# Optimization experiments

Measured on AMD Instinct MI355X. Metric: run time of the kernel, lower is better.

Reference implementation:

```python
import jax, jax.numpy as jnp
import numpy as np

B, DIM, IN_DIM, H, W = 4, 256, 128, 128, 128
DD = IN_DIM // 2          # down_dim = 64
HEADS = 8
BN_EPS = 1e-5


def conv2d(x, w, b=None, pad=0, dil=1):
    y = jax.lax.conv_general_dilated(
        x, w, window_strides=(1, 1),
        padding=[(pad, pad), (pad, pad)],
        rhs_dilation=(dil, dil),
        dimension_numbers=('NCHW', 'OIHW', 'NCHW'))
    if b is not None:
        y = y + b[None, :, None, None]
    return y


def bn_relu(x, s, o):
    # eval-mode BatchNorm2d with running_mean=0, running_var=1
    return jax.nn.relu(x * (s / np.sqrt(1.0 + BN_EPS))[None, :, None, None] + o[None, :, None, None])


def setup_inputs() -> dict:
    ks = iter(jax.random.split(jax.random.key(0), 80))

    def w(shape, sc=0.05):
        return sc * jax.random.normal(next(ks), shape, jnp.float32)

    def s(c):
        return 1.0 + 0.1 * jax.random.normal(next(ks), (c,), jnp.float32)

    def o(c):
        return 0.02 * jax.random.normal(next(ks), (c,), jnp.float32)

    d = {}
    d['x'] = jax.random.normal(next(ks), (B, DIM, H, W), jnp.float32)
    d['w_dc'] = w((IN_DIM, DIM, 3, 3)); d['b_dc'] = w((IN_DIM,)); d['s_dc'] = s(IN_DIM); d['o_dc'] = o(IN_DIM)
    d['w1'] = w((DD, IN_DIM, 1, 1)); d['b1'] = w((DD,)); d['s1'] = s(DD); d['o1'] = o(DD)
    d['w2'] = w((DD, DD, 3, 3)); d['b2'] = w((DD,)); d['s2'] = s(DD); d['o2'] = o(DD)
    d['w3'] = w((DD, DD, 3, 3)); d['b3'] = w((DD,)); d['s3'] = s(DD); d['o3'] = o(DD)
    d['w4'] = w((DD, DD, 3, 3)); d['b4'] = w((DD,)); d['s4'] = s(DD); d['o4'] = o(DD)
    d['w5'] = w((DD, IN_DIM, 1, 1)); d['b5'] = w((DD,)); d['s5'] = s(DD); d['o5'] = o(DD)
    d['temperature'] = jnp.ones((HEADS, 1, 1), jnp.float32)
    d['w_po'] = w((DD, 2 * DD, 1, 1))  # project_out, bias=False
    d['w_wa'] = w((DD // 16, DD, 1, 1)); d['b_wa'] = w((DD // 16,)); d['s_wa'] = s(DD // 16); d['o_wa'] = o(DD // 16)
    d['w_wb'] = w((DD, DD // 16, 1, 1)); d['b_wb'] = w((DD,))
    d['w_f'] = w((DD, 5 * DD, 1, 1)); d['b_f'] = w((DD,)); d['s_f'] = s(DD); d['o_f'] = o(DD)
    d['w_oa'] = w((DD // 2, DD, 3, 3)); d['b_oa'] = w((DD // 2,)); d['s_oa'] = s(DD // 2); d['o_oa'] = o(DD // 2)
    d['w_ob'] = w((1, DD // 2, 1, 1)); d['b_ob'] = w((1,))
    return d


def reference(x, w_dc, b_dc, s_dc, o_dc, w1, b1, s1, o1, w2, b2, s2, o2,
              w3, b3, s3, o3, w4, b4, s4, o4, w5, b5, s5, o5,
              temperature, w_po, w_wa, b_wa, s_wa, o_wa, w_wb, b_wb,
              w_f, b_f, s_f, o_f, w_oa, b_oa, s_oa, o_oa, w_ob, b_ob):

    def branch(c):
        b, ch, h, wd = c.shape
        f = jnp.fft.fft2(c)                                   # [b,ch,h,w] complex64 (q=k=v=tepqkv)
        qkv = f.reshape(b, HEADS, ch // HEADS, h * wd)        # v (unnormalized)
        n = jnp.sqrt(jnp.sum(jnp.square(jnp.abs(qkv)), axis=-1, keepdims=True))
        qn = qkv / jnp.maximum(n, 1e-12)                      # F.normalize(dim=-1); q == k
        attn = jnp.einsum('bhcn,bhdn->bhcd', qn, qn) * temperature
        # custom complex normalization: separate real/imag softmax
        attn = jax.lax.complex(jax.nn.softmax(attn.real, axis=-1),
                               jax.nn.softmax(attn.imag, axis=-1))
        of = jnp.abs(jnp.fft.ifft2(jnp.einsum('bhcd,bhdn->bhcn', attn, qkv)))  # ifft2 over (c, hw)
        of = of.reshape(b, ch, h, wd)
        g = jax.nn.sigmoid(conv2d(bn_relu(conv2d(f.real, w_wa, b_wa), s_wa, o_wa), w_wb, b_wb))
        ol = jnp.abs(jnp.fft.ifft2(g * f))                    # ifft2 over (h, w)
        return conv2d(jnp.concatenate([of, ol], axis=1), w_po) + c

    xd = bn_relu(conv2d(x, w_dc, b_dc, pad=1), s_dc, o_dc)
    c1 = bn_relu(conv2d(xd, w1, b1), s1, o1)
    c2 = bn_relu(conv2d(c1, w2, b2, pad=3, dil=3), s2, o2)
    F2 = branch(c2)
    c3 = bn_relu(conv2d(c1 + F2, w3, b3, pad=5, dil=5), s3, o3)
    F3 = branch(c3)
    c4 = bn_relu(conv2d(c1 + F3, w4, b4, pad=7, dil=7), s4, o4)
    F4 = branch(c4)
    # conv5: global avg pool -> 1x1 conv -> bilinear upsample of a 1x1 map == broadcast
    c5 = bn_relu(conv2d(jnp.mean(xd, axis=(2, 3), keepdims=True), w5, b5), s5, o5)
    c5 = jnp.broadcast_to(c5, (c5.shape[0], c5.shape[1], xd.shape[2], xd.shape[3]))
    fused = bn_relu(conv2d(jnp.concatenate([c1, F2, F3, F4, c5], axis=1), w_f, b_f), s_f, o_f)
    return conv2d(bn_relu(conv2d(fused, w_oa, b_oa, pad=1), s_oa, o_oa), w_ob, b_ob)
```

## Files before the change

### kernel.cpp

```cpp
#include <hip/hip_runtime.h>

#define S 16384
#define PI_F 3.14159265358979f

struct Ptrs { const float* p[43]; };

enum : int {
  O_SBDC=0, O_SB1=256, O_SB2=512, O_SB3=768, O_SB4=1024, O_SB5=1280,
  O_SBWA=1536, O_SBF=1792, O_SBOA=2048,
  O_M=2304, O_C5=2816, O_NRM=3072, O_GRAM=3328, O_ATT2=7424, O_BEFF=11520,
  O_WB=16384,
  O_PART=147456,
  O_H=180224,
  O_WP=442368,
  O_A=524288,
  O_FIN=8912896,
  O_CC=25690112,
  O_DRE=29884416, O_DIMG=34078720,
  O_ERE=38273024, O_EIM=42467328,
  O_G=46661632
};

typedef short bfrag __attribute__((ext_vector_type(8)));
typedef float ffrag __attribute__((ext_vector_type(4)));

__device__ __forceinline__ float bf2f(unsigned short u){
  union { unsigned int i; float f; } v; v.i = ((unsigned int)u) << 16; return v.f;
}
__device__ __forceinline__ unsigned short f2bf(float f){
  unsigned int x = __float_as_uint(f);
  unsigned int r = x + 0x7fffu + ((x >> 16) & 1u);
  return (unsigned short)(r >> 16);
}

__global__ void prep_sb_kernel(Ptrs P, float* ws){
  const float r = rsqrtf(1.0f + 1e-5f);
  int bi=0, si=0, oi=0, C=0, dst=0;
  switch (blockIdx.x){
    case 0: bi=2; si=3; oi=4; C=128; dst=O_SBDC; break;
    case 1: bi=6; si=7; oi=8; C=64; dst=O_SB1; break;
    case 2: bi=10; si=11; oi=12; C=64; dst=O_SB2; break;
    case 3: bi=14; si=15; oi=16; C=64; dst=O_SB3; break;
    case 4: bi=18; si=19; oi=20; C=64; dst=O_SB4; break;
    case 5: bi=22; si=23; oi=24; C=64; dst=O_SB5; break;
    case 6: bi=28; si=29; oi=30; C=4;  dst=O_SBWA; break;
    case 7: bi=34; si=35; oi=36; C=64; dst=O_SBF; break;
    default: bi=38; si=39; oi=40; C=32; dst=O_SBOA; break;
  }
  for (int c = threadIdx.x; c < C; c += 256){
    float bb = P.p[bi][c], ss = P.p[si][c], oo = P.p[oi][c];
    float sc = ss * r;
    ws[dst + c] = sc;
    ws[dst + C + c] = bb * sc + oo;
  }
}

__global__ __launch_bounds__(256) void xpad_kernel(const float* __restrict__ x,
    unsigned short* __restrict__ XT){
  int yy = blockIdx.x, b = blockIdx.y;
  long obase = ((long)(b*130) + yy) * (130L*256);
  int tid = threadIdx.x;
  if (yy == 0 || yy == 129){
    uint4 z; z.x=0; z.y=0; z.z=0; z.w=0;
    for (int i = tid; i < 130*256/8; i += 256)
      *(uint4*)(XT + obase + (long)i*8) = z;
    return;
  }
  __shared__ float LT[64][129];
  int y = yy - 1;
  for (int c0 = 0; c0 < 256; c0 += 64){
    for (int idx = tid; idx < 64*128; idx += 256){
      int ci = idx >> 7, xx = idx & 127;
      LT[ci][xx] = x[((long)(b*256 + c0 + ci)*128 + y)*128 + xx];
    }
    __syncthreads();
    for (int idx = tid; idx < 128*16; idx += 256){
      int xp = idx >> 4, c4 = (idx & 15)*4;
      ushort4 v;
      v.x = f2bf(LT[c4][xp]);   v.y = f2bf(LT[c4+1][xp]);
      v.z = f2bf(LT[c4+2][xp]); v.w = f2bf(LT[c4+3][xp]);
      *(ushort4*)(XT + obase + (long)(xp+1)*256 + c0 + c4) = v;
    }
    __syncthreads();
  }
  if (tid < 64){
    ushort4 z; z.x=0; z.y=0; z.z=0; z.w=0;
    *(ushort4*)(XT + obase + tid*4) = z;
    *(ushort4*)(XT + obase + 129L*256 + tid*4) = z;
  }
}

__global__ void wt_kernel(const float* __restrict__ w, unsigned short* __restrict__ WH,
    unsigned short* __restrict__ WL){
  for (int e = blockIdx.x*256 + threadIdx.x; e < 294912; e += gridDim.x*256){
    int c32 = e & 31, co = (e >> 5) & 127, kc = (e >> 12) & 7, sh = e >> 15;
    int ky = sh / 3, kx = sh - ky*3;
    int ci = kc*32 + c32;
    float v = w[((long)(co*256 + ci)*3 + ky)*3 + kx];
    unsigned short h = f2bf(v);
    WH[e] = h;
    WL[e] = f2bf(v - bf2f(h));
  }
}

__global__ void wtg_kernel(Ptrs P, unsigned short* __restrict__ WB){
  const float* w; int cout; long off;
  switch (blockIdx.y){
    case 0: w = P.p[9];  cout = 64; off = 0;      break;
    case 1: w = P.p[13]; cout = 64; off = 73728;  break;
    case 2: w = P.p[17]; cout = 64; off = 147456; break;
    default: w = P.p[37]; cout = 32; off = 221184; break;
  }
  int total = 576*cout;
  unsigned short* WH = WB + off;
  unsigned short* WL = WH + total;
  for (int e = blockIdx.x*256 + threadIdx.x; e < total; e += gridDim.x*256){
    int c32 = e & 31;
    int co = (e >> 5) & (cout - 1);
    int kc = (e / (32*cout)) & 1;
    int sh = e / (64*cout);
    int ky = sh/3, kx = sh - ky*3;
    int ci = kc*32 + c32;
    float v = w[((long)(co*64 + ci)*3 + ky)*3 + kx];
    unsigned short h = f2bf(v);
    WH[e] = h;
    WL[e] = f2bf(v - bf2f(h));
  }
}

__global__ void wtp_kernel(Ptrs P, unsigned short* __restrict__ WP){
  const float* w; int KC, wstr; long off;
  switch (blockIdx.y){
    case 0: w = P.p[5];  KC = 4; wstr = 128; off = 0;     break;
    case 1: w = P.p[26]; KC = 4; wstr = 128; off = 16384; break;
    default: w = P.p[33]; KC = 8; wstr = 320; off = 32768; break;
  }
  int total = KC*64*32;
  unsigned short* WH = WP + off;
  unsigned short* WL = WH + total;
  for (int e = blockIdx.x*256 + threadIdx.x; e < total; e += gridDim.x*256){
    int c32 = e & 31, co = (e >> 5) & 63, kc = e >> 11;
    float v = w[(long)co*wstr + kc*32 + c32];
    unsigned short h = f2bf(v);
    WH[e] = h;
    WL[e] = f2bf(v - bf2f(h));
  }
}

template<int DIL>
__global__ __launch_bounds__(256) void xpad64_kernel(const float* __restrict__ in1,
    const float* __restrict__ in2, long in_bs, unsigned short* __restrict__ XP){
  constexpr int TW = 128 + 2*DIL;
  int yy = blockIdx.x, b = blockIdx.y;
  long obase = (long)(b*TW + yy) * TW * 64;
  int tid = threadIdx.x;
  if (yy < DIL || yy >= 128 + DIL){
    uint4 z; z.x=0; z.y=0; z.z=0; z.w=0;
    for (int i = tid; i < TW*8; i += 256)
      *(uint4*)(XP + obase + (long)i*8) = z;
    return;
  }
  __shared__ float LT[64][129];
  int y = yy - DIL;
  const float* p1 = in1 + (long)b*in_bs + (long)y*128;
  const float* p2 = in2 ? in2 + (long)b*in_bs + (long)y*128 : nullptr;
  for (int idx = tid; idx < 64*128; idx += 256){
    int ci = idx >> 7, xx = idx & 127;
    float v = p1[(long)ci*S + xx];
    if (p2) v += p2[(long)ci*S + xx];
    LT[ci][xx] = v;
  }
  __syncthreads();
  for (int i = tid; i < 2*DIL*16; i += 256){
    int side = i / (DIL*16);
    int r = i - side*(DIL*16);
    int xcol = side ? (128 + DIL + (r >> 4)) : (r >> 4);
    ushort4 z; z.x=0; z.y=0; z.z=0; z.w=0;
    *(ushort4*)(XP + obase + (long)xcol*64 + (r & 15)*4) = z;
  }
  for (int idx = tid; idx < 128*16; idx += 256){
    int xp = idx >> 4, c4 = (idx & 15)*4;
    ushort4 v;
    v.x = f2bf(LT[c4][xp]);   v.y = f2bf(LT[c4+1][xp]);
    v.z = f2bf(LT[c4+2][xp]); v.w = f2bf(LT[c4+3][xp]);
    *(ushort4*)(XP + obase + (long)(xp + DIL)*64 + c4) = v;
  }
}

template<int DIL, int KC, int NBLK>
__global__ __launch_bounds__(256) void conv3x3_mfma_kernel(
    const unsigned short* __restrict__ XP,
    const unsigned short* __restrict__ WH, const unsigned short* __restrict__ WL,
    const float* __restrict__ scbi, float* __restrict__ out){
  constexpr int CIN = KC*32;
  constexpr int TW = 128 + 2*DIL;
  constexpr int STEPS = 9*KC;
  constexpr int MI = (NBLK == 64) ? 4 : 2;
  constexpr int LDA = 36;
  __shared__ unsigned short Als[128*LDA];
  __shared__ unsigned short BHs[NBLK*LDA];
  __shared__ unsigned short BLs[NBLK*LDA];
  int bid = blockIdx.x;
  int y = (bid & 7)*16 + ((bid >> 3) & 15);
  int b = (bid >> 7) & 3;
  int n2 = bid >> 9;
  int nb = gridDim.x >> 9; if (nb == 0) nb = 1;
  int coutTotal = nb * NBLK;
  int tid = threadIdx.x, wv = tid >> 6, lane = tid & 63;
  int mt0 = (NBLK == 64) ? (wv & 1)*4 : wv*2;
  int nt0 = (NBLK == 64) ? (wv >> 1)*2 : 0;
  ffrag acc[MI][2];
  #pragma unroll
  for (int i = 0; i < MI; i++)
    #pragma unroll
    for (int j = 0; j < 2; j++)
      #pragma unroll
      for (int r = 0; r < 4; r++) acc[i][j][r] = 0.f;

  int pixq = tid >> 2, qq = tid & 3;
  int kq = (lane >> 4)*8, rown = lane & 15;
  int wrA0 = pixq*LDA + qq*8;
  int wrA1 = (pixq + 64)*LDA + qq*8;
  int wrB  = (tid >> 2)*LDA + qq*8;

  uint4 A0, A1, BHr, BLr;
  {
    long abase = ((long)(b*TW + y)*TW)*CIN + qq*8;
    A0 = *(const uint4*)(XP + abase + (long)pixq*CIN);
    A1 = *(const uint4*)(XP + abase + (long)(pixq + 64)*CIN);
    long gw = (long)n2*NBLK*32;
    if (NBLK == 64 || tid < 128){
      BHr = *(const uint4*)(WH + gw + tid*8);
      BLr = *(const uint4*)(WL + gw + tid*8);
    }
  }
  for (int step = 0; step < STEPS; step++){
    __syncthreads();
    *(uint4*)&Als[wrA0] = A0;
    *(uint4*)&Als[wrA1] = A1;
    if (NBLK == 64 || tid < 128){
      *(uint4*)&BHs[wrB] = BHr;
      *(uint4*)&BLs[wrB] = BLr;
    }
    __syncthreads();
    if (step + 1 < STEPS){
      int s2 = step + 1;
      int sh = s2 / KC, kc = s2 - sh*KC;
      int ky = sh / 3, kx = sh - ky*3;
      long abase = ((long)(b*TW + y + ky*DIL)*TW + kx*DIL)*CIN + kc*32 + qq*8;
      A0 = *(const uint4*)(XP + abase + (long)pixq*CIN);
      A1 = *(const uint4*)(XP + abase + (long)(pixq + 64)*CIN);
      long gw = ((long)s2*coutTotal + n2*NBLK)*32;
      if (NBLK == 64 || tid < 128){
        BHr = *(const uint4*)(WH + gw + tid*8);
        BLr = *(const uint4*)(WL + gw + tid*8);
      }
    }
    bfrag af[MI], bhf[2], blf[2];
    #pragma unroll
    for (int i = 0; i < MI; i++)
      af[i] = *(const bfrag*)&Als[((mt0 + i)*16 + rown)*LDA + kq];
    #pragma unroll
    for (int j = 0; j < 2; j++){
      bhf[j] = *(const bfrag*)&BHs[((nt0 + j)*16 + rown)*LDA + kq];
      blf[j] = *(const bfrag*)&BLs[((nt0 + j)*16 + rown)*LDA + kq];
    }
    #pragma unroll
    for (int i = 0; i < MI; i++)
      #pragma unroll
      for (int j = 0; j < 2; j++){
        acc[i][j] = __builtin_amdgcn_mfma_f32_16x16x32_bf16(af[i], blf[j], acc[i][j], 0, 0, 0);
        acc[i][j] = __builtin_amdgcn_mfma_f32_16x16x32_bf16(af[i], bhf[j], acc[i][j], 0, 0, 0);
      }
  }
  #pragma unroll
  for (int i = 0; i < MI; i++){
    int pixel = (mt0 + i)*16 + (lane >> 4)*4;
    #pragma unroll
    for (int j = 0; j < 2; j++){
      int co = n2*NBLK + (nt0 + j)*16 + (lane & 15);
      float sc = scbi[co], bb = scbi[coutTotal + co];
      float* op = out + ((long)(b*coutTotal + co))*S + y*128 + pixel;
      #pragma unroll
      for (int r = 0; r < 4; r++)
        op[r] = fmaxf(acc[i][j][r]*sc + bb, 0.f);
    }
  }
}

template<int MODE, int KC, int BF16IN>
__global__ __launch_bounds__(256) void conv1x1_mfma_kernel(
    const void* __restrict__ inv, long in_bs,
    const unsigned short* __restrict__ WH, const unsigned short* __restrict__ WL,
    const float* __restrict__ scbi, const float* __restrict__ beff,
    const float* __restrict__ res, long res_bs,
    float* __restrict__ out, long out_bs){
  constexpr int LDA = 36;
  __shared__ unsigned short Als[128*LDA];
  __shared__ unsigned short BHs[64*LDA];
  __shared__ unsigned short BLs[64*LDA];
  int bid = blockIdx.x;
  int y = (bid & 7)*16 + ((bid >> 3) & 15);
  int b = bid >> 7;
  int tid = threadIdx.x, wv = tid >> 6, lane = tid & 63;
  int mt0 = (wv & 1)*4, nt0 = (wv >> 1)*2;
  ffrag acc[4][2];
  #pragma unroll
  for (int i = 0; i < 4; i++)
    #pragma unroll
    for (int j = 0; j < 2; j++)
      #pragma unroll
      for (int r = 0; r < 4; r++) acc[i][j][r] = 0.f;
  int pq = tid & 31, cg = tid >> 5;
  int kq = (lane >> 4)*8, rown = lane & 15;
  int wrB = (tid >> 2)*LDA + (tid & 3)*8;
  const float* ibf = (const float*)inv + (long)b*in_bs + y*128;
  const unsigned short* ibs = (const unsigned short*)inv + (long)b*in_bs + y*128;
  unsigned short a[16];
  uint4 BHr, BLr;
  #pragma unroll
  for (int cc = 0; cc < 4; cc++)
    #pragma unroll
    for (int i = 0; i < 4; i++){
      if (BF16IN) a[cc*4 + i] = ibs[(long)(cg*4 + cc)*S + pq + 32*i];
      else        a[cc*4 + i] = f2bf(ibf[(long)(cg*4 + cc)*S + pq + 32*i]);
    }
  BHr = *(const uint4*)(WH + tid*8);
  BLr = *(const uint4*)(WL + tid*8);
  for (int kc = 0; kc < KC; kc++){
    __syncthreads();
    #pragma unroll
    for (int i = 0; i < 4; i++){
      ushort4 v;
      v.x = a[0 + i];  v.y = a[4 + i];
      v.z = a[8 + i];  v.w = a[12 + i];
      *(ushort4*)&Als[(pq + 32*i)*LDA + cg*4] = v;
    }
    *(uint4*)&BHs[wrB] = BHr;
    *(uint4*)&BLs[wrB] = BLr;
    __syncthreads();
    if (kc + 1 < KC){
      #pragma unroll
      for (int cc = 0; cc < 4; cc++)
        #pragma unroll
        for (int i = 0; i < 4; i++){
          long off = (long)((kc + 1)*32 + cg*4 + cc)*S + pq + 32*i;
          if (BF16IN) a[cc*4 + i] = ibs[off];
          else        a[cc*4 + i] = f2bf(ibf[off]);
        }
      long gw = (long)(kc + 1)*2048;
      BHr = *(const uint4*)(WH + gw + tid*8);
      BLr = *(const uint4*)(WL + gw + tid*8);
    }
    bfrag af[4], bhf[2], blf[2];
    #pragma unroll
    for (int i = 0; i < 4; i++)
      af[i] = *(const bfrag*)&Als[((mt0 + i)*16 + rown)*LDA + kq];
    #pragma unroll
    for (int j = 0; j < 2; j++){
      bhf[j] = *(const bfrag*)&BHs[((nt0 + j)*16 + rown)*LDA + kq];
      blf[j] = *(const bfrag*)&BLs[((nt0 + j)*16 + rown)*LDA + kq];
    }
    #pragma unroll
    for (int i = 0; i < 4; i++)
      #pragma unroll
      for (int j = 0; j < 2; j++){
        acc[i][j] = __builtin_amdgcn_mfma_f32_16x16x32_bf16(af[i], blf[j], acc[i][j], 0, 0, 0);
        acc[i][j] = __builtin_amdgcn_mfma_f32_16x16x32_bf16(af[i], bhf[j], acc[i][j], 0, 0, 0);
      }
  }
  #pragma unroll
  for (int i = 0; i < 4; i++){
    int pixel = (mt0 + i)*16 + (lane >> 4)*4;
    #pragma unroll
    for (int j = 0; j < 2; j++){
      int co = (nt0 + j)*16 + (lane & 15);
      float* op = out + (long)b*out_bs + (long)co*S + y*128 + pixel;
      #pragma unroll
      for (int r = 0; r < 4; r++){
        float v = acc[i][j][r];
        if (MODE == 0){
          v = fmaxf(v*scbi[co] + scbi[64 + co], 0.f);
        } else if (MODE == 1){
          v += res[(long)b*res_bs + (long)co*S + y*128 + pixel + r];
        } else {
          v = fmaxf(v*scbi[co] + beff[b*64 + co], 0.f);
        }
        op[r] = v;
      }
    }
  }
}

__device__ __forceinline__ void fft128_mk_tw(float (&tws)[8], float (&twc)[8],
                                             float sign, int lane){
  float a0 = sign * (2.0f*PI_F/128.0f) * (float)lane;
  __sincosf(a0, &tws[0], &twc[0]);
  int i = 1;
  #pragma unroll
  for (int h = 32; h >= 1; h >>= 1, i++){
    int j = lane & (h - 1);
    float a = sign * (2.0f*PI_F/128.0f) * (float)(j * (64/h));
    __sincosf(a, &tws[i], &twc[i]);
  }
}

__device__ __forceinline__ void fft128(float& z0r, float& z0i, float& z1r, float& z1i,
    const float (&tws)[8], const float (&twc)[8], int lane){
  {
    float ar = z0r, ai = z0i, br = z1r, bi = z1i;
    z0r = ar + br; z0i = ai + bi;
    float dr = ar - br, di = ai - bi;
    float s = tws[0], c = twc[0];
    z1r = dr*c - di*s; z1i = dr*s + di*c;
  }
  int idx = 1;
  #pragma unroll
  for (int h = 32; h >= 1; h >>= 1, idx++){
    float s = tws[idx], c = twc[idx];
    bool up = (lane & h) != 0;
    float pr, pi, nr, ni;
    pr = __shfl_xor(z0r, h, 64); pi = __shfl_xor(z0i, h, 64);
    if (!up){ nr = z0r + pr; ni = z0i + pi; }
    else { float dr = pr - z0r, di = pi - z0i; nr = dr*c - di*s; ni = dr*s + di*c; }
    z0r = nr; z0i = ni;
    pr = __shfl_xor(z1r, h, 64); pi = __shfl_xor(z1i, h, 64);
    if (!up){ nr = z1r + pr; ni = z1i + pi; }
    else { float dr = pr - z1r, di = pi - z1i; nr = dr*c - di*s; ni = dr*s + di*c; }
    z1r = nr; z1i = ni;
  }
}


__global__ __launch_bounds__(1024) void fft2_fwd_kernel(const float* __restrict__ in,
    unsigned short* __restrict__ outRe, unsigned short* __restrict__ outIm){
  __shared__ float lre[128][129];
  __shared__ float lim[128][129];
  int plane = blockIdx.x;
  int tid = threadIdx.x, wv = tid >> 6, lane = tid & 63;
  long pbase = (long)plane * S;
  for (int i = tid; i < S/4; i += 1024){
    int px = i*4; int r = px >> 7, c = px & 127;
    float4 v = *(const float4*)(in + pbase + px);
    lre[r][c] = v.x; lre[r][c+1] = v.y; lre[r][c+2] = v.z; lre[r][c+3] = v.w;
  }
  float tws[8], twc[8];
  fft128_mk_tw(tws, twc, -1.0f, lane);
  __syncthreads();
  #pragma unroll
  for (int rr = 0; rr < 8; rr++){
    int r = wv*8 + rr;
    float z0r = lre[r][lane], z0i = 0.f;
    float z1r = lre[r][lane + 64], z1i = 0.f;
    fft128(z0r, z0i, z1r, z1i, tws, twc, lane);
    int k = __brev(lane) >> 25;
    lre[r][k] = z0r;     lim[r][k] = z0i;
    lre[r][k+1] = z1r;   lim[r][k+1] = z1i;
  }
  __syncthreads();
  #pragma unroll
  for (int cc = 0; cc < 8; cc++){
    int c = wv*8 + cc;
    float z0r = lre[lane][c], z0i = lim[lane][c];
    float z1r = lre[lane + 64][c], z1i = lim[lane + 64][c];
    fft128(z0r, z0i, z1r, z1i, tws, twc, lane);
    int k = __brev(lane) >> 25;
    lre[k][c] = z0r;     lim[k][c] = z0i;
    lre[k+1][c] = z1r;   lim[k+1][c] = z1i;
  }
  __syncthreads();
  for (int i = tid; i < S/2; i += 1024){
    int px = i*2; int r = px >> 7, c = px & 127;
    ushort2 vr, vi;
    vr.x = f2bf(lre[r][c]); vr.y = f2bf(lre[r][c+1]);
    vi.x = f2bf(lim[r][c]); vi.y = f2bf(lim[r][c+1]);
    *(ushort2*)(outRe + pbase + px) = vr;
    *(ushort2*)(outIm + pbase + px) = vi;
  }
}

__global__ __launch_bounds__(1024) void ifft2_gate_abs_ol_kernel(
    const unsigned short* __restrict__ Dre, const unsigned short* __restrict__ Dim,
    const float* __restrict__ H, const float* __restrict__ wb, const float* __restrict__ bwb,
    unsigned short* __restrict__ AB){
  __shared__ float lre[128][129];
  __shared__ float lim[128][129];
  int plane = blockIdx.x;
  int b = plane >> 6, ch = plane & 63;
  int tid = threadIdx.x, wv = tid >> 6, lane = tid & 63;
  long pbase = (long)plane * S;
  float w0 = wb[ch*4], w1 = wb[ch*4+1], w2 = wb[ch*4+2], w3 = wb[ch*4+3];
  float bw = bwb[ch];
  const float* Hb = H + (long)b*4*S;
  for (int i = tid; i < S; i += 1024){
    int r = i >> 7, c = i & 127;
    float hv = bw + w0*Hb[i] + w1*Hb[S + i] + w2*Hb[2*S + i] + w3*Hb[3*S + i];
    float g = 1.0f / (1.0f + __expf(-hv));
    lre[r][c] = bf2f(Dre[pbase + i]) * g;
    lim[r][c] = bf2f(Dim[pbase + i]) * g;
  }
  float tws[8], twc[8];
  fft128_mk_tw(tws, twc, 1.0f, lane);
  __syncthreads();
  #pragma unroll
  for (int cc = 0; cc < 8; cc++){
    int c = wv*8 + cc;
    float z0r = lre[lane][c], z0i = lim[lane][c];
    float z1r = lre[lane + 64][c], z1i = lim[lane + 64][c];
    fft128(z0r, z0i, z1r, z1i, tws, twc, lane);
    int k = __brev(lane) >> 25;
    lre[k][c] = z0r;     lim[k][c] = z0i;
    lre[k+1][c] = z1r;   lim[k+1][c] = z1i;
  }
  __syncthreads();
  unsigned short* out = AB + ((long)(b*128 + 64 + ch)) * S;
  #pragma unroll
  for (int rr = 0; rr < 8; rr++){
    int r = wv*8 + rr;
    float z0r = lre[r][lane], z0i = lim[r][lane];
    float z1r = lre[r][lane + 64], z1i = lim[r][lane + 64];
    fft128(z0r, z0i, z1r, z1i, tws, twc, lane);
    int k = __brev(lane) >> 25;
    ushort2 v;
    v.x = f2bf(sqrtf(z0r*z0r + z0i*z0i) * (1.0f/16384.0f));
    v.y = f2bf(sqrtf(z1r*z1r + z1i*z1i) * (1.0f/16384.0f));
    *(ushort2*)(out + (long)r*128 + k) = v;
  }
}

__global__ __launch_bounds__(1024) void ifft2_abs_ofT_kernel(
    const unsigned short* __restrict__ Ere, const unsigned short* __restrict__ Eim,
    unsigned short* __restrict__ AB){
  __shared__ float lre[128][129];
  __shared__ float lim[128][129];
  int plane = blockIdx.x;
  int b = plane >> 6, ch = plane & 63;
  int tid = threadIdx.x, wv = tid >> 6, lane = tid & 63;
  long pbase = (long)plane * S;
  for (int i = tid; i < S; i += 1024){
    int r = i >> 7, c = i & 127;
    lre[r][c] = bf2f(Ere[pbase + i]);
    lim[r][c] = bf2f(Eim[pbase + i]);
  }
  float tws[8], twc[8];
  fft128_mk_tw(tws, twc, 1.0f, lane);
  __syncthreads();
  #pragma unroll
  for (int cc = 0; cc < 8; cc++){
    int c = wv*8 + cc;
    float z0r = lre[lane][c], z0i = lim[lane][c];
    float z1r = lre[lane + 64][c], z1i = lim[lane + 64][c];
    fft128(z0r, z0i, z1r, z1i, tws, twc, lane);
    int k = __brev(lane) >> 25;
    float s, co;
    float a0 = (2.0f*PI_F/16384.0f) * (float)(c * k);
    __sincosf(a0, &s, &co);
    float t = z0r*co - z0i*s; z0i = z0r*s + z0i*co; z0r = t;
    float a1 = (2.0f*PI_F/16384.0f) * (float)(c * (k + 1));
    __sincosf(a1, &s, &co);
    t = z1r*co - z1i*s; z1i = z1r*s + z1i*co; z1r = t;
    lre[k][c] = z0r;     lim[k][c] = z0i;
    lre[k+1][c] = z1r;   lim[k+1][c] = z1i;
  }
  __syncthreads();
  float absv[8][2];
  #pragma unroll
  for (int rr = 0; rr < 8; rr++){
    int r = wv*8 + rr;
    float z0r = lre[r][lane], z0i = lim[r][lane];
    float z1r = lre[r][lane + 64], z1i = lim[r][lane + 64];
    fft128(z0r, z0i, z1r, z1i, tws, twc, lane);
    absv[rr][0] = sqrtf(z0r*z0r + z0i*z0i) * (1.0f/16384.0f);
    absv[rr][1] = sqrtf(z1r*z1r + z1i*z1i) * (1.0f/16384.0f);
  }
  __syncthreads();
  int k2 = __brev(lane) >> 25;
  #pragma unroll
  for (int rr = 0; rr < 8; rr++){
    int r = wv*8 + rr;
    lre[k2][r] = absv[rr][0];
    lre[k2+1][r] = absv[rr][1];
  }
  __syncthreads();
  unsigned short* out = AB + ((long)(b*128 + ch)) * S;
  for (int i = tid; i < S/2; i += 1024){
    int px = i*2; int r = px >> 7, c = px & 127;
    ushort2 v;
    v.x = f2bf(lre[r][c]); v.y = f2bf(lre[r][c+1]);
    *(ushort2*)(out + px) = v;
  }
}

__global__ __launch_bounds__(256) void gram_part_kernel(
    const unsigned short* __restrict__ Dre, const unsigned short* __restrict__ Dim,
    float* __restrict__ PART){
  int bh = blockIdx.x, slab = blockIdx.y;
  long base = (long)bh * 8 * S;
  int n0 = slab * 2048;
  float accr[36], acci[36], nsq[8];
  #pragma unroll
  for (int i = 0; i < 36; i++){ accr[i] = 0.f; acci[i] = 0.f; }
  #pragma unroll
  for (int i = 0; i < 8; i++) nsq[i] = 0.f;
  for (int it = 0; it < 8; it++){
    int n = n0 + it*256 + threadIdx.x;
    float xr[8], xi[8];
    #pragma unroll
    for (int c = 0; c < 8; c++){
      xr[c] = bf2f(Dre[base + (long)c*S + n]);
      xi[c] = bf2f(Dim[base + (long)c*S + n]);
      nsq[c] += xr[c]*xr[c] + xi[c]*xi[c];
    }
    int t = 0;
    #pragma unroll
    for (int c = 0; c < 8; c++)
      #pragma unroll
      for (int d = c; d < 8; d++){
        accr[t] += xr[c]*xr[d] - xi[c]*xi[d];
        acci[t] += xr[c]*xi[d] + xi[c]*xr[d];
        t++;
      }
  }
  __shared__ float red[4][80];
  int wv = threadIdx.x >> 6, lane = threadIdx.x & 63;
  #pragma unroll
  for (int i = 0; i < 80; i++){
    float v = (i < 36) ? accr[i] : (i < 72) ? acci[i - 36] : nsq[i - 72];
    #pragma unroll
    for (int o = 32; o; o >>= 1) v += __shfl_xor(v, o, 64);
    if (lane == 0) red[wv][i] = v;
  }
  __syncthreads();
  if (threadIdx.x < 80){
    int i = threadIdx.x;
    PART[(long)(bh*8 + slab)*80 + i] = red[0][i] + red[1][i] + red[2][i] + red[3][i];
  }
}

__global__ void attn2f_kernel(const float* __restrict__ PART,
    const float* __restrict__ temp, float* __restrict__ ATT2){
  __shared__ float ssum[80];
  __shared__ float sar[64], sai[64];
  int bh = blockIdx.x;
  int t = threadIdx.x;
  if (t < 80){
    float s = 0.f;
    for (int i = 0; i < 8; i++) s += PART[(long)(bh*8 + i)*80 + t];
    ssum[t] = s;
  }
  __syncthreads();
  if (t >= 64) return;
  int lane = t;
  int c = lane >> 3, d = lane & 7;
  int lo = min(c, d), hi = max(c, d);
  int t2 = lo*8 - lo*(lo - 1)/2 + (hi - lo);
  float nnc = fmaxf(sqrtf(ssum[72 + c]), 1e-12f);
  float nnd = fmaxf(sqrtf(ssum[72 + d]), 1e-12f);
  float inv = temp[bh & 7] / (nnc * nnd);
  float ar = ssum[t2] * inv, ai = ssum[36 + t2] * inv;
  float m = ar;
  m = fmaxf(m, __shfl_xor(m, 1, 64)); m = fmaxf(m, __shfl_xor(m, 2, 64)); m = fmaxf(m, __shfl_xor(m, 4, 64));
  float e = __expf(ar - m);
  float su = e;
  su += __shfl_xor(su, 1, 64); su += __shfl_xor(su, 2, 64); su += __shfl_xor(su, 4, 64);
  ar = e / su;
  m = ai;
  m = fmaxf(m, __shfl_xor(m, 1, 64)); m = fmaxf(m, __shfl_xor(m, 2, 64)); m = fmaxf(m, __shfl_xor(m, 4, 64));
  e = __expf(ai - m);
  su = e;
  su += __shfl_xor(su, 1, 64); su += __shfl_xor(su, 2, 64); su += __shfl_xor(su, 4, 64);
  ai = e / su;
  sar[lane] = ar; sai[lane] = ai;
  __syncthreads();
  const float ct[8] = {1.f, 0.70710678f, 0.f, -0.70710678f, -1.f, -0.70710678f, 0.f, 0.70710678f};
  const float st[8] = {0.f, 0.70710678f, 1.f, 0.70710678f, 0.f, -0.70710678f, -1.f, -0.70710678f};
  int cp = c;
  float sr = 0.f, si = 0.f;
  #pragma unroll
  for (int cc = 0; cc < 8; cc++){
    int k = (cc * cp) & 7;
    float a = sar[cc*8 + d], b2 = sai[cc*8 + d];
    sr += ct[k]*a - st[k]*b2;
    si += ct[k]*b2 + st[k]*a;
  }
  float2 v; v.x = sr * 0.125f; v.y = si * 0.125f;
  ((float2*)ATT2)[bh*64 + lane] = v;
}

__global__ __launch_bounds__(256) void apply_attn_kernel(
    const unsigned short* __restrict__ Dre, const unsigned short* __restrict__ Dim,
    const float* __restrict__ ATT2,
    unsigned short* __restrict__ Ere, unsigned short* __restrict__ Eim){
  int bh = blockIdx.y;
  int px = blockIdx.x*1024 + (threadIdx.x & 63)*4 + (threadIdx.x >> 6)*256;
  long base = (long)bh * 8 * S + px;
  float4 ar[8], ai[8];
  #pragma unroll
  for (int i = 0; i < 8; i++){
    ar[i].x = ar[i].y = ar[i].z = ar[i].w = 0.f;
    ai[i].x = ai[i].y = ai[i].z = ai[i].w = 0.f;
  }
  #pragma unroll
  for (int d = 0; d < 8; d++){
    ushort4 ur = *(const ushort4*)(Dre + base + (long)d*S);
    ushort4 ui = *(const ushort4*)(Dim + base + (long)d*S);
    float4 xr, xi;
    xr.x = bf2f(ur.x); xr.y = bf2f(ur.y); xr.z = bf2f(ur.z); xr.w = bf2f(ur.w);
    xi.x = bf2f(ui.x); xi.y = bf2f(ui.y); xi.z = bf2f(ui.z); xi.w = bf2f(ui.w);
    #pragma unroll
    for (int cp = 0; cp < 8; cp++){
      float wr = ATT2[bh*128 + (cp*8 + d)*2];
      float wi = ATT2[bh*128 + (cp*8 + d)*2 + 1];
      ar[cp].x += wr*xr.x - wi*xi.x;  ai[cp].x += wr*xi.x + wi*xr.x;
      ar[cp].y += wr*xr.y - wi*xi.y;  ai[cp].y += wr*xi.y + wi*xr.y;
      ar[cp].z += wr*xr.z - wi*xi.z;  ai[cp].z += wr*xi.z + wi*xr.z;
      ar[cp].w += wr*xr.w - wi*xi.w;  ai[cp].w += wr*xi.w + wi*xr.w;
    }
  }
  #pragma unroll
  for (int cp = 0; cp < 8; cp++){
    ushort4 vr, vi;
    vr.x = f2bf(ar[cp].x); vr.y = f2bf(ar[cp].y); vr.z = f2bf(ar[cp].z); vr.w = f2bf(ar[cp].w);
    vi.x = f2bf(ai[cp].x); vi.y = f2bf(ai[cp].y); vi.z = f2bf(ai[cp].z); vi.w = f2bf(ai[cp].w);
    *(ushort4*)(Ere + base + (long)cp*S) = vr;
    *(ushort4*)(Eim + base + (long)cp*S) = vi;
  }
}

__global__ __launch_bounds__(256) void gateh_kernel(const unsigned short* __restrict__ Dre,
    const float* __restrict__ wa, const float* __restrict__ sbwa, float* __restrict__ H){
  int b = blockIdx.y;
  int px = blockIdx.x*256 + threadIdx.x;
  long base = (long)b * 64 * S + px;
  float h0 = 0.f, h1 = 0.f, h2 = 0.f, h3 = 0.f;
  for (int ci = 0; ci < 64; ci++){
    float x = bf2f(Dre[base + (long)ci*S]);
    h0 += wa[ci]*x; h1 += wa[64 + ci]*x; h2 += wa[128 + ci]*x; h3 += wa[192 + ci]*x;
  }
  long ob = (long)b * 4 * S + px;
  H[ob]       = fmaxf(h0*sbwa[0] + sbwa[4], 0.f);
  H[ob + S]   = fmaxf(h1*sbwa[1] + sbwa[5], 0.f);
  H[ob + 2*S] = fmaxf(h2*sbwa[2] + sbwa[6], 0.f);
  H[ob + 3*S] = fmaxf(h3*sbwa[3] + sbwa[7], 0.f);
}

__global__ __launch_bounds__(256) void mean_kernel(const float* __restrict__ A, float* __restrict__ M){
  int p = blockIdx.x;
  long base = (long)p * S;
  float s = 0.f;
  for (int n = threadIdx.x; n < S; n += 256) s += A[base + n];
  #pragma unroll
  for (int o = 32; o; o >>= 1) s += __shfl_xor(s, o, 64);
  __shared__ float sm[4];
  if ((threadIdx.x & 63) == 0) sm[threadIdx.x >> 6] = s;
  __syncthreads();
  if (threadIdx.x == 0) M[p] = (sm[0] + sm[1] + sm[2] + sm[3]) * (1.0f/16384.0f);
}

__global__ void c5_kernel(const float* __restrict__ W5, const float* __restrict__ sb5,
    const float* __restrict__ M, float* __restrict__ C5){
  int t = threadIdx.x;
  if (t >= 256) return;
  int b = t >> 6, co = t & 63;
  float s = 0.f;
  for (int ci = 0; ci < 128; ci++) s += W5[co*128 + ci] * M[b*128 + ci];
  C5[t] = fmaxf(s * sb5[co] + sb5[64 + co], 0.f);
}

__global__ void beff_kernel(const float* __restrict__ WF, const float* __restrict__ sbf,
    const float* __restrict__ C5, float* __restrict__ BEFF){
  int t = threadIdx.x;
  if (t >= 256) return;
  int b = t >> 6, co = t & 63;
  float s = 0.f;
  for (int j = 0; j < 64; j++) s += WF[co*320 + 256 + j] * C5[b*64 + j];
  BEFF[t] = s * sbf[co] + sbf[64 + co];
}

__global__ __launch_bounds__(256) void ob_kernel(const float* __restrict__ Tin,
    const float* __restrict__ wob, const float* __restrict__ bob, float* __restrict__ out){
  int b = blockIdx.y;
  int px = blockIdx.x*1024 + (threadIdx.x & 63)*4 + (threadIdx.x >> 6)*256;
  float b0 = bob[0];
  float4 a; a.x = b0; a.y = b0; a.z = b0; a.w = b0;
  for (int ci = 0; ci < 32; ci++){
    float4 v = *(const float4*)(Tin + ((long)b*32 + ci)*S + px);
    float w = wob[ci];
    a.x += w*v.x; a.y += w*v.y; a.z += w*v.z; a.w += w*v.w;
  }
  *(float4*)(out + (long)b*S + px) = a;
}

extern "C" void kernel_launch(void* const* d_in, const int* in_sizes, int n_in,
                              void* d_out, int out_size, void* d_ws, size_t ws_size,
                              hipStream_t stream){
  float* ws = (float*)d_ws;
  Ptrs P;
  for (int i = 0; i < 43 && i < n_in; i++) P.p[i] = (const float*)d_in[i];
  float* out = (float*)d_out;

  float* A   = ws + O_A;
  float* FIN = ws + O_FIN;
  float* CC  = ws + O_CC;
  float* G   = ws + O_G;
  float* H   = ws + O_H;

  unsigned short* DRE16 = (unsigned short*)(ws + O_DRE);
  unsigned short* DIM16 = (unsigned short*)(ws + O_DIMG);
  unsigned short* ERE16 = (unsigned short*)(ws + O_ERE);
  unsigned short* EIM16 = (unsigned short*)(ws + O_EIM);
  unsigned short* AB    = (unsigned short*)(ws + O_A);

  unsigned short* XT  = (unsigned short*)(ws + O_DRE);
  unsigned short* WHd = (unsigned short*)(ws + O_CC);
  unsigned short* WLd = (unsigned short*)(ws + O_CC + 147456);
  unsigned short* WB  = (unsigned short*)(ws + O_WB);
  unsigned short* WP  = (unsigned short*)(ws + O_WP);
  unsigned short* XP  = (unsigned short*)(ws + O_ERE);

  prep_sb_kernel<<<dim3(9), dim3(256), 0, stream>>>(P, ws);
  xpad_kernel<<<dim3(130, 4), dim3(256), 0, stream>>>(P.p[0], XT);
  wt_kernel<<<dim3(128), dim3(256), 0, stream>>>(P.p[1], WHd, WLd);
  wtg_kernel<<<dim3(16, 4), dim3(256), 0, stream>>>(P, WB);
  wtp_kernel<<<dim3(8, 3), dim3(256), 0, stream>>>(P, WP);

  conv3x3_mfma_kernel<1,8,64><<<dim3(1024), dim3(256), 0, stream>>>(
      XT, WHd, WLd, ws + O_SBDC, A);

  mean_kernel<<<dim3(512), dim3(256), 0, stream>>>(A, ws + O_M);
  c5_kernel<<<dim3(1), dim3(256), 0, stream>>>(P.p[21], ws + O_SB5, ws + O_M, ws + O_C5);
  beff_kernel<<<dim3(1), dim3(256), 0, stream>>>(P.p[33], ws + O_SBF, ws + O_C5, ws + O_BEFF);

  conv1x1_mfma_kernel<0,4,0><<<dim3(512), dim3(256), 0, stream>>>(
      A, 128*S, WP, WP + 8192, ws + O_SB1, nullptr, nullptr, 0, FIN, 256*S);

  for (int k = 0; k < 3; k++){
    const float* sb = ws + (k == 0 ? O_SB2 : k == 1 ? O_SB3 : O_SB4);
    const float* in2 = (k == 0) ? nullptr : FIN + (long)(64*k)*S;
    unsigned short* wh = WB + (k == 0 ? 0 : k == 1 ? 73728 : 147456);
    if (k == 0){
      xpad64_kernel<3><<<dim3(134, 4), dim3(256), 0, stream>>>(FIN, in2, 256*S, XP);
      conv3x3_mfma_kernel<3,2,64><<<dim3(512), dim3(256), 0, stream>>>(
          XP, wh, wh + 36864, sb, CC);
    } else if (k == 1){
      xpad64_kernel<5><<<dim3(138, 4), dim3(256), 0, stream>>>(FIN, in2, 256*S, XP);
      conv3x3_mfma_kernel<5,2,64><<<dim3(512), dim3(256), 0, stream>>>(
          XP, wh, wh + 36864, sb, CC);
    } else {
      xpad64_kernel<7><<<dim3(142, 4), dim3(256), 0, stream>>>(FIN, in2, 256*S, XP);
      conv3x3_mfma_kernel<7,2,64><<<dim3(512), dim3(256), 0, stream>>>(
          XP, wh, wh + 36864, sb, CC);
    }

    fft2_fwd_kernel<<<dim3(256), dim3(1024), 0, stream>>>(CC, DRE16, DIM16);
    gram_part_kernel<<<dim3(32, 8), dim3(256), 0, stream>>>(DRE16, DIM16, ws + O_PART);
    attn2f_kernel<<<dim3(32), dim3(128), 0, stream>>>(ws + O_PART, P.p[25], ws + O_ATT2);
    gateh_kernel<<<dim3(64, 4), dim3(256), 0, stream>>>(DRE16, P.p[27], ws + O_SBWA, H);
    ifft2_gate_abs_ol_kernel<<<dim3(256), dim3(1024), 0, stream>>>(
        DRE16, DIM16, H, P.p[31], P.p[32], AB);
    apply_attn_kernel<<<dim3(16, 32), dim3(256), 0, stream>>>(DRE16, DIM16, ws + O_ATT2, ERE16, EIM16);
    ifft2_abs_ofT_kernel<<<dim3(256), dim3(1024), 0, stream>>>(ERE16, EIM16, AB);
    conv1x1_mfma_kernel<1,4,1><<<dim3(512), dim3(256), 0, stream>>>(
        AB, 128*S, WP + 16384, WP + 24576, nullptr, nullptr, CC, 64*S,
        FIN + (long)(64*(k + 1))*S, 256*S);
  }

  conv1x1_mfma_kernel<2,8,0><<<dim3(512), dim3(256), 0, stream>>>(
      FIN, 256*S, WP + 32768, WP + 49152, ws + O_SBF, ws + O_BEFF, nullptr, 0, CC, 64*S);
  xpad64_kernel<1><<<dim3(130, 4), dim3(256), 0, stream>>>(CC, nullptr, 64*S, XP);
  conv3x3_mfma_kernel<1,2,32><<<dim3(512), dim3(256), 0, stream>>>(
      XP, WB + 221184, WB + 221184 + 18432, ws + O_SBOA, G);
  ob_kernel<<<dim3(16, 4), dim3(256), 0, stream>>>(G, P.p[41], P.p[42], out);
}
```

Before: 909.4 us.

## Restructure 3x3 conv to reuse padded row tile across kx; fuse attention apply into ifft

The 3x3 MFMA conv now loads one full padded input row (TW pixels) per ky/kc into LDS and reuses it for all three kx taps. Weights are read straight from global memory into registers instead of being staged in LDS. The dilated 64-channel convs switch to 32-channel output blocks with twice as many blocks. Separately, the attention-apply kernel is folded into the ifft2 kernel, so the bf16 E intermediates are no longer written and read back. The cost is recomputing the 8-way complex mix per plane, which reads 8 D planes per output plane, plus uncached per-wave weight loads.

```diff
diff --git a/kernel.cpp b/kernel.cpp
--- a/kernel.cpp
+++ b/kernel.cpp
@@ -194,12 +194,9 @@
     const float* __restrict__ scbi, float* __restrict__ out){
   constexpr int CIN = KC*32;
   constexpr int TW = 128 + 2*DIL;
-  constexpr int STEPS = 9*KC;
-  constexpr int MI = (NBLK == 64) ? 4 : 2;
+  constexpr int NJ = NBLK/32;
   constexpr int LDA = 36;
-  __shared__ unsigned short Als[128*LDA];
-  __shared__ unsigned short BHs[NBLK*LDA];
-  __shared__ unsigned short BLs[NBLK*LDA];
+  __shared__ unsigned short As[TW*LDA];
   int bid = blockIdx.x;
   int y = (bid & 7)*16 + ((bid >> 3) & 15);
   int b = (bid >> 7) & 3;
@@ -207,78 +204,61 @@
   int nb = gridDim.x >> 9; if (nb == 0) nb = 1;
   int coutTotal = nb * NBLK;
   int tid = threadIdx.x, wv = tid >> 6, lane = tid & 63;
-  int mt0 = (NBLK == 64) ? (wv & 1)*4 : wv*2;
-  int nt0 = (NBLK == 64) ? (wv >> 1)*2 : 0;
-  ffrag acc[MI][2];
-  #pragma unroll
-  for (int i = 0; i < MI; i++)
-    #pragma unroll
-    for (int j = 0; j < 2; j++)
+  int mhalf = wv & 1, nhalf = wv >> 1;
+  int px0 = mhalf*64;
+  ffrag acc[4][NJ];
+  #pragma unroll
+  for (int i = 0; i < 4; i++)
+    #pragma unroll
+    for (int j = 0; j < NJ; j++)
       #pragma unroll
       for (int r = 0; r < 4; r++) acc[i][j][r] = 0.f;
 
-  int pixq = tid >> 2, qq = tid & 3;
   int kq = (lane >> 4)*8, rown = lane & 15;
-  int wrA0 = pixq*LDA + qq*8;
-  int wrA1 = (pixq + 64)*LDA + qq*8;
-  int wrB  = (tid >> 2)*LDA + qq*8;
-
-  uint4 A0, A1, BHr, BLr;
-  {
-    long abase = ((long)(b*TW + y)*TW)*CIN + qq*8;
-    A0 = *(const uint4*)(XP + abase + (long)pixq*CIN);
-    A1 = *(const uint4*)(XP + abase + (long)(pixq + 64)*CIN);
-    long gw = (long)n2*NBLK*32;
-    if (NBLK == 64 || tid < 128){
-      BHr = *(const uint4*)(WH + gw + tid*8);
-      BLr = *(const uint4*)(WL + gw + tid*8);
-    }
-  }
-  for (int step = 0; step < STEPS; step++){
-    __syncthreads();
-    *(uint4*)&Als[wrA0] = A0;
-    *(uint4*)&Als[wrA1] = A1;
-    if (NBLK == 64 || tid < 128){
-      *(uint4*)&BHs[wrB] = BHr;
-      *(uint4*)&BLs[wrB] = BLr;
-    }
-    __syncthreads();
-    if (step + 1 < STEPS){
-      int s2 = step + 1;
-      int sh = s2 / KC, kc = s2 - sh*KC;
-      int ky = sh / 3, kx = sh - ky*3;
-      long abase = ((long)(b*TW + y + ky*DIL)*TW + kx*DIL)*CIN + kc*32 + qq*8;
-      A0 = *(const uint4*)(XP + abase + (long)pixq*CIN);
-      A1 = *(const uint4*)(XP + abase + (long)(pixq + 64)*CIN);
-      long gw = ((long)s2*coutTotal + n2*NBLK)*32;
-      if (NBLK == 64 || tid < 128){
-        BHr = *(const uint4*)(WH + gw + tid*8);
-        BLr = *(const uint4*)(WL + gw + tid*8);
+  int sx = tid >> 2, sq = tid & 3;
+  int cobase = n2*NBLK + nhalf*(NBLK/2);
+
+  for (int ky = 0; ky < 3; ky++){
+    long rowbase = ((long)(b*TW + y + ky*DIL))*TW*CIN;
+    for (int kc = 0; kc < KC; kc++){
+      __syncthreads();
+      for (int x = sx; x < TW; x += 64){
+        uint4 v = *(const uint4*)(XP + rowbase + (long)x*CIN + kc*32 + sq*8);
+        *(uint4*)&As[x*LDA + sq*8] = v;
       }
-    }
-    bfrag af[MI], bhf[2], blf[2];
-    #pragma unroll
-    for (int i = 0; i < MI; i++)
-      af[i] = *(const bfrag*)&Als[((mt0 + i)*16 + rown)*LDA + kq];
-    #pragma unroll
-    for (int j = 0; j < 2; j++){
-      bhf[j] = *(const bfrag*)&BHs[((nt0 + j)*16 + rown)*LDA + kq];
-      blf[j] = *(const bfrag*)&BLs[((nt0 + j)*16 + rown)*LDA + kq];
-    }
-    #pragma unroll
-    for (int i = 0; i < MI; i++)
+      __syncthreads();
       #pragma unroll
-      for (int j = 0; j < 2; j++){
-        acc[i][j] = __builtin_amdgcn_mfma_f32_16x16x32_bf16(af[i], blf[j], acc[i][j], 0, 0, 0);
-        acc[i][j] = __builtin_amdgcn_mfma_f32_16x16x32_bf16(af[i], bhf[j], acc[i][j], 0, 0, 0);
+      for (int kx = 0; kx < 3; kx++){
+        int step = (ky*3 + kx)*KC + kc;
+        bfrag bhf[NJ], blf[NJ];
+        #pragma unroll
+        for (int j = 0; j < NJ; j++){
+          long wb = ((long)step*coutTotal + cobase + j*16 + rown)*32 + kq;
+          bhf[j] = *(const bfrag*)(WH + wb);
+          blf[j] = *(const bfrag*)(WL + wb);
+        }
+        bfrag af[4];
+        #pragma unroll
+        for (int i = 0; i < 4; i++){
+          int x = px0 + i*16 + rown + kx*DIL;
+          af[i] = *(const bfrag*)&As[x*LDA + kq];
+        }
+        #pragma unroll
+        for (int i = 0; i < 4; i++)
+          #pragma unroll
+          for (int j = 0; j < NJ; j++){
+            acc[i][j] = __builtin_amdgcn_mfma_f32_16x16x32_bf16(af[i], blf[j], acc[i][j], 0, 0, 0);
+            acc[i][j] = __builtin_amdgcn_mfma_f32_16x16x32_bf16(af[i], bhf[j], acc[i][j], 0, 0, 0);
+          }
       }
-  }
-  #pragma unroll
-  for (int i = 0; i < MI; i++){
-    int pixel = (mt0 + i)*16 + (lane >> 4)*4;
-    #pragma unroll
-    for (int j = 0; j < 2; j++){
-      int co = n2*NBLK + (nt0 + j)*16 + (lane & 15);
+    }
+  }
+  #pragma unroll
+  for (int i = 0; i < 4; i++){
+    int pixel = px0 + i*16 + (lane >> 4)*4;
+    #pragma unroll
+    for (int j = 0; j < NJ; j++){
+      int co = cobase + j*16 + (lane & 15);
       float sc = scbi[co], bb = scbi[coutTotal + co];
       float* op = out + ((long)(b*coutTotal + co))*S + y*128 + pixel;
       #pragma unroll
@@ -528,19 +508,38 @@
   }
 }
 
-__global__ __launch_bounds__(1024) void ifft2_abs_ofT_kernel(
-    const unsigned short* __restrict__ Ere, const unsigned short* __restrict__ Eim,
-    unsigned short* __restrict__ AB){
+__global__ __launch_bounds__(1024) void ifft2_attn_abs_ofT_kernel(
+    const unsigned short* __restrict__ Dre, const unsigned short* __restrict__ Dim,
+    const float* __restrict__ ATT2, unsigned short* __restrict__ AB){
   __shared__ float lre[128][129];
   __shared__ float lim[128][129];
   int plane = blockIdx.x;
   int b = plane >> 6, ch = plane & 63;
+  int bh = plane >> 3;
+  int cp = plane & 7;
   int tid = threadIdx.x, wv = tid >> 6, lane = tid & 63;
-  long pbase = (long)plane * S;
-  for (int i = tid; i < S; i += 1024){
-    int r = i >> 7, c = i & 127;
-    lre[r][c] = bf2f(Ere[pbase + i]);
-    lim[r][c] = bf2f(Eim[pbase + i]);
+  long hbase = (long)bh * 8 * S;
+  float wr[8], wi[8];
+  #pragma unroll
+  for (int d = 0; d < 8; d++){
+    wr[d] = ATT2[bh*128 + (cp*8 + d)*2];
+    wi[d] = ATT2[bh*128 + (cp*8 + d)*2 + 1];
+  }
+  for (int i = tid; i < S/2; i += 1024){
+    int px = i*2;
+    float sr0=0.f, si0=0.f, sr1=0.f, si1=0.f;
+    #pragma unroll
+    for (int d = 0; d < 8; d++){
+      ushort2 ur = *(const ushort2*)(Dre + hbase + (long)d*S + px);
+      ushort2 ui = *(const ushort2*)(Dim + hbase + (long)d*S + px);
+      float xr0 = bf2f(ur.x), xi0 = bf2f(ui.x);
+      float xr1 = bf2f(ur.y), xi1 = bf2f(ui.y);
+      sr0 += wr[d]*xr0 - wi[d]*xi0;  si0 += wr[d]*xi0 + wi[d]*xr0;
+      sr1 += wr[d]*xr1 - wi[d]*xi1;  si1 += wr[d]*xi1 + wi[d]*xr1;
+    }
+    int r = px >> 7, c = px & 127;
+    lre[r][c] = sr0;   lim[r][c] = si0;
+    lre[r][c+1] = sr1; lim[r][c+1] = si1;
   }
   float tws[8], twc[8];
   fft128_mk_tw(tws, twc, 1.0f, lane);
@@ -687,46 +686,6 @@
   ((float2*)ATT2)[bh*64 + lane] = v;
 }
 
-__global__ __launch_bounds__(256) void apply_attn_kernel(
-    const unsigned short* __restrict__ Dre, const unsigned short* __restrict__ Dim,
-    const float* __restrict__ ATT2,
-    unsigned short* __restrict__ Ere, unsigned short* __restrict__ Eim){
-  int bh = blockIdx.y;
-  int px = blockIdx.x*1024 + (threadIdx.x & 63)*4 + (threadIdx.x >> 6)*256;
-  long base = (long)bh * 8 * S + px;
-  float4 ar[8], ai[8];
-  #pragma unroll
-  for (int i = 0; i < 8; i++){
-    ar[i].x = ar[i].y = ar[i].z = ar[i].w = 0.f;
-    ai[i].x = ai[i].y = ai[i].z = ai[i].w = 0.f;
-  }
-  #pragma unroll
-  for (int d = 0; d < 8; d++){
-    ushort4 ur = *(const ushort4*)(Dre + base + (long)d*S);
-    ushort4 ui = *(const ushort4*)(Dim + base + (long)d*S);
-    float4 xr, xi;
-    xr.x = bf2f(ur.x); xr.y = bf2f(ur.y); xr.z = bf2f(ur.z); xr.w = bf2f(ur.w);
-    xi.x = bf2f(ui.x); xi.y = bf2f(ui.y); xi.z = bf2f(ui.z); xi.w = bf2f(ui.w);
-    #pragma unroll
-    for (int cp = 0; cp < 8; cp++){
-      float wr = ATT2[bh*128 + (cp*8 + d)*2];
-      float wi = ATT2[bh*128 + (cp*8 + d)*2 + 1];
-      ar[cp].x += wr*xr.x - wi*xi.x;  ai[cp].x += wr*xi.x + wi*xr.x;
-      ar[cp].y += wr*xr.y - wi*xi.y;  ai[cp].y += wr*xi.y + wi*xr.y;
-      ar[cp].z += wr*xr.z - wi*xi.z;  ai[cp].z += wr*xi.z + wi*xr.z;
-      ar[cp].w += wr*xr.w - wi*xi.w;  ai[cp].w += wr*xi.w + wi*xr.w;
-    }
-  }
-  #pragma unroll
-  for (int cp = 0; cp < 8; cp++){
-    ushort4 vr, vi;
-    vr.x = f2bf(ar[cp].x); vr.y = f2bf(ar[cp].y); vr.z = f2bf(ar[cp].z); vr.w = f2bf(ar[cp].w);
-    vi.x = f2bf(ai[cp].x); vi.y = f2bf(ai[cp].y); vi.z = f2bf(ai[cp].z); vi.w = f2bf(ai[cp].w);
-    *(ushort4*)(Ere + base + (long)cp*S) = vr;
-    *(ushort4*)(Eim + base + (long)cp*S) = vi;
-  }
-}
-
 __global__ __launch_bounds__(256) void gateh_kernel(const unsigned short* __restrict__ Dre,
     const float* __restrict__ wa, const float* __restrict__ sbwa, float* __restrict__ H){
   int b = blockIdx.y;
@@ -807,8 +766,6 @@
 
   unsigned short* DRE16 = (unsigned short*)(ws + O_DRE);
   unsigned short* DIM16 = (unsigned short*)(ws + O_DIMG);
-  unsigned short* ERE16 = (unsigned short*)(ws + O_ERE);
-  unsigned short* EIM16 = (unsigned short*)(ws + O_EIM);
   unsigned short* AB    = (unsigned short*)(ws + O_A);
 
   unsigned short* XT  = (unsigned short*)(ws + O_DRE);
@@ -840,15 +797,15 @@
     unsigned short* wh = WB + (k == 0 ? 0 : k == 1 ? 73728 : 147456);
     if (k == 0){
       xpad64_kernel<3><<<dim3(134, 4), dim3(256), 0, stream>>>(FIN, in2, 256*S, XP);
-      conv3x3_mfma_kernel<3,2,64><<<dim3(512), dim3(256), 0, stream>>>(
+      conv3x3_mfma_kernel<3,2,32><<<dim3(1024), dim3(256), 0, stream>>>(
           XP, wh, wh + 36864, sb, CC);
     } else if (k == 1){
       xpad64_kernel<5><<<dim3(138, 4), dim3(256), 0, stream>>>(FIN, in2, 256*S, XP);
-      conv3x3_mfma_kernel<5,2,64><<<dim3(512), dim3(256), 0, stream>>>(
+      conv3x3_mfma_kernel<5,2,32><<<dim3(1024), dim3(256), 0, stream>>>(
           XP, wh, wh + 36864, sb, CC);
     } else {
       xpad64_kernel<7><<<dim3(142, 4), dim3(256), 0, stream>>>(FIN, in2, 256*S, XP);
-      conv3x3_mfma_kernel<7,2,64><<<dim3(512), dim3(256), 0, stream>>>(
+      conv3x3_mfma_kernel<7,2,32><<<dim3(1024), dim3(256), 0, stream>>>(
           XP, wh, wh + 36864, sb, CC);
     }
 
@@ -858,8 +815,8 @@
     gateh_kernel<<<dim3(64, 4), dim3(256), 0, stream>>>(DRE16, P.p[27], ws + O_SBWA, H);
     ifft2_gate_abs_ol_kernel<<<dim3(256), dim3(1024), 0, stream>>>(
         DRE16, DIM16, H, P.p[31], P.p[32], AB);
-    apply_attn_kernel<<<dim3(16, 32), dim3(256), 0, stream>>>(DRE16, DIM16, ws + O_ATT2, ERE16, EIM16);
-    ifft2_abs_ofT_kernel<<<dim3(256), dim3(1024), 0, stream>>>(ERE16, EIM16, AB);
+    ifft2_attn_abs_ofT_kernel<<<dim3(256), dim3(1024), 0, stream>>>(
+        DRE16, DIM16, ws + O_ATT2, AB);
     conv1x1_mfma_kernel<1,4,1><<<dim3(512), dim3(256), 0, stream>>>(
         AB, 128*S, WP + 16384, WP + 24576, nullptr, nullptr, CC, 64*S,
         FIN + (long)(64*(k + 1))*S, 256*S);
```

Result: no change. 921.7 us (+1.4%).
